# Performance work log

Hardware: AMD Instinct MI355X
Metric: run time of the kernel (lower is better)

Reference implementation:

```python
import jax, jax.numpy as jnp
import numpy as np

CELU_ALPHA = 0.1  # torchani standard CELU alpha


def _celu(x):
    return jax.nn.celu(x, alpha=CELU_ALPHA)


def setup_inputs() -> dict:
    key = jax.random.key(0)
    ks = jax.random.split(key, 12)
    N, S, E, D = 20000, 4, 8, 1008
    dims = [D, 256, 192, 160, 1]
    inp = {
        "aev": jax.random.normal(ks[0], (N, D), jnp.float32),
        "species": jax.random.randint(ks[1], (N,), 0, S, dtype=jnp.int64),
    }
    for l in range(4):
        din, dout = dims[l], dims[l + 1]
        inp[f"W{l}"] = jax.random.normal(ks[2 + 2 * l], (S, E, din, dout), jnp.float32) * (1.0 / np.sqrt(din).astype(np.float32))
        inp[f"b{l}"] = jax.random.normal(ks[3 + 2 * l], (S, E, dout), jnp.float32) * 0.05
    return inp


def reference(aev, species, W0, b0, W1, b1, W2, b2, W3, b3):
    # Faithful math of InferModel.forward: for each species i, gather atoms of
    # that species, run the BmmAtomicNetwork (ensemble of MLPs via bmm, CELU
    # activations, mean over ensemble members), sum per-species energies, then
    # sum into a single [1]-shaped total energy.
    # JIT-friendly equivalent: evaluate every species network on all atoms
    # (S=4 is small) and select each atom's output by its species index.
    # h: [S, E, N, hidden]
    h = _celu(jnp.einsum('ni,seio->seno', aev, W0) + b0[:, :, None, :])
    h = _celu(jnp.einsum('seni,seio->seno', h, W1) + b1[:, :, None, :])
    h = _celu(jnp.einsum('seni,seio->seno', h, W2) + b2[:, :, None, :])
    h = jnp.einsum('seni,seio->seno', h, W3) + b3[:, :, None, :]  # [S,E,N,1]
    per_atom = h.mean(axis=1)[:, :, 0]  # mean over ensemble -> [S, N]
    sel = jnp.take_along_axis(per_atom, species[None, :], axis=0)[0]  # [N]
    return jnp.sum(sel, keepdims=True)  # shape [1], total energy
```

## Files before the change

### kernel.cpp

```cpp
#include <hip/hip_runtime.h>
#include <cmath>

#define NA 20000
#define NS 4
#define NE 8
#define DD 1008
#define BM 128
#define MAXT 157
#define MAXROWS 20608

typedef unsigned short u16;
typedef unsigned int u32;
typedef unsigned long long u64;
typedef u16 u16x8 __attribute__((ext_vector_type(8)));
typedef u16 u16x4 __attribute__((ext_vector_type(4)));
typedef float f32x4 __attribute__((ext_vector_type(4)));
typedef short s16x8 __attribute__((ext_vector_type(8)));

__device__ __forceinline__ float bf2f(u16 h) {
  u32 u = ((u32)h) << 16;
  return __builtin_bit_cast(float, u);
}
__device__ __forceinline__ u16 f2bf(float f) {
  u32 b = __builtin_bit_cast(u32, f);
  u32 lsb = (b >> 16) & 1;
  return (u16)((b + 0x7fffu + lsb) >> 16);
}
__device__ __forceinline__ float celu_f(float x) {
  return x > 0.f ? x : 0.1f * expm1f(10.f * x);
}
__device__ __forceinline__ float gf(const void* g, size_t i, bool isF32) {
  return isF32 ? ((const float*)g)[i] : bf2f(((const u16*)g)[i]);
}

__device__ __forceinline__ void gll16(const void* g, const u16* lds) {
#if __has_builtin(__builtin_amdgcn_global_load_lds)
  __builtin_amdgcn_global_load_lds(
      (const __attribute__((address_space(1))) u32*)g,
      (__attribute__((address_space(3))) u32*)(u16*)lds, 16, 0, 0);
#else
  int l = threadIdx.x & 63;
  *(f32x4*)((u16*)lds + l * 8) = *(const f32x4*)g;
#endif
}

__global__ void k_initprobe(const void* __restrict__ aev, const void* __restrict__ species,
                            int* __restrict__ w) {
  __shared__ int sh[2];
  int tid = threadIdx.x;
  if (tid < 32) w[tid] = 0;
  if (tid == 0) { sh[0] = 0; sh[1] = 0; }
  __syncthreads();
  const u16* a = (const u16*)aev;
  int bad = 0;
  for (int i = 0; i < 16; ++i) {
    u16 h = a[tid * 16 + i];
    int ex = (h >> 7) & 0xFF;
    if (ex < 107 || ex > 147) ++bad;
  }
  atomicAdd(&sh[0], bad);
  const int* sp = (const int*)species;
  int odd = 0;
  for (int i = 0; i < 4; ++i)
    if (sp[(tid * 4 + i) * 2 + 1] != 0) ++odd;
  atomicAdd(&sh[1], odd);
  __syncthreads();
  if (tid == 0) {
    w[18] = (sh[0] > 400) ? 1 : 0;
    w[19] = (sh[1] == 0) ? 1 : 0;
  }
}

__device__ __forceinline__ int get_species(const void* sp, int i, bool i64) {
  int s = i64 ? ((const int*)sp)[2 * i] : ((const int*)sp)[i];
  return s < 0 ? 0 : (s > 3 ? 3 : s);
}

__global__ void k_count(const void* __restrict__ species, int* __restrict__ w) {
  int i = blockIdx.x * 256 + threadIdx.x;
  int lane = threadIdx.x & 63;
  int s = (i < NA) ? get_species(species, i, w[19] != 0) : -1;
  for (int sp = 0; sp < 4; ++sp) {
    u64 m = __ballot(s == sp);
    if (m != 0 && lane == (__ffsll((long long)m) - 1))
      atomicAdd(&w[sp], __popcll(m));
  }
}

__global__ void k_scan(int* w) {
  int b = 0, pb = 0;
  for (int s = 0; s < 4; ++s) {
    w[13 + s] = b; b += w[s];
    w[20 + s] = pb; pb += ((w[s] + 127) >> 7) << 7;
  }
  w[24] = pb;
}

__global__ void k_scatter(const void* __restrict__ species, int* __restrict__ w,
                          int* __restrict__ order) {
  int i = blockIdx.x * 256 + threadIdx.x;
  int lane = threadIdx.x & 63;
  int s = (i < NA) ? get_species(species, i, w[19] != 0) : -1;
  for (int sp = 0; sp < 4; ++sp) {
    u64 m = __ballot(s == sp);
    if (m == 0) continue;
    int leader = __ffsll((long long)m) - 1;
    int base = 0;
    if (lane == leader) base = atomicAdd(&w[4 + sp], __popcll(m));
    base = __shfl(base, leader);
    if (s == sp) {
      int rank = __popcll(m & ((lane == 63) ? 0x7fffffffffffffffULL : ((1ULL << lane) - 1)));
      order[w[13 + sp] + base + rank] = i;
    }
  }
}

__global__ void k_gather(const void* __restrict__ aev, const int* __restrict__ w,
                         const int* __restrict__ order, u16* __restrict__ aevb) {
  const bool isF32 = (w[18] != 0);
  const int t = threadIdx.x;
  const int r = blockIdx.x * 4 + (t >> 7);
  const int j = t & 127;
  if (j >= 126) return;
  const int s = (r >= w[21]) + (r >= w[22]) + (r >= w[23]);
  const int local = r - w[20 + s];
  u16x8 v = {0, 0, 0, 0, 0, 0, 0, 0};
  if (local < w[s]) {
    const int src = order[w[13 + s] + local];
    if (isF32) {
      const float* p = (const float*)aev + (size_t)src * DD + j * 8;
      const f32x4 f0 = *(const f32x4*)p;
      const f32x4 f1 = *(const f32x4*)(p + 4);
#pragma unroll
      for (int i = 0; i < 4; ++i) { v[i] = f2bf(f0[i]); v[4 + i] = f2bf(f1[i]); }
    } else {
      v = *(const u16x8*)((const u16*)aev + (size_t)src * DD + j * 8);
    }
  }
  *(u16x8*)(aevb + (size_t)r * DD + j * 8) = v;
}

__global__ void k_tr(const void* __restrict__ W, u16* __restrict__ out,
                     int K, int N, int Kpad, const int* __restrict__ w) {
  __shared__ u16 tile[64][68];
  const bool isF32 = (w[18] != 0);
  int se = blockIdx.x, k0 = blockIdx.y * 64, n0 = blockIdx.z * 64;
  int t = threadIdx.x;
  const size_t inBase = (size_t)se * K * N;
#pragma unroll
  for (int c = 0; c < 4; ++c) {
    int kk = (t >> 4) + c * 16, nn = (t & 15) * 4;
    int k = k0 + kk, n = n0 + nn;
    u16x4 v = {0, 0, 0, 0};
    if (k < K && n < N) {
      if (isF32) {
        f32x4 f = *(const f32x4*)((const float*)W + inBase + (size_t)k * N + n);
        v[0] = f2bf(f[0]); v[1] = f2bf(f[1]); v[2] = f2bf(f[2]); v[3] = f2bf(f[3]);
      } else {
        v = *(const u16x4*)((const u16*)W + inBase + (size_t)k * N + n);
      }
    }
    *(u16x4*)(&tile[kk][nn]) = v;
  }
  __syncthreads();
  int nloc = t >> 2, ks = (t & 3) * 16;
  if (n0 + nloc < N) {
    u16x8 o0, o1;
#pragma unroll
    for (int i = 0; i < 8; ++i) { o0[i] = tile[ks + i][nloc]; o1[i] = tile[ks + 8 + i][nloc]; }
    size_t ob = (size_t)se * N * Kpad + (size_t)(n0 + nloc) * Kpad + k0 + ks;
    *(u16x8*)(out + ob) = o0;
    *(u16x8*)(out + ob + 8) = o1;
  }
}

__global__ void k_small(const void* b0, const void* b1, const void* b2, const void* b3,
                        const void* W3, u16* ob0, u16* ob1, u16* ob2, u16* ob3, u16* oW3,
                        u16* gap, const int* __restrict__ w) {
  const bool isF32 = (w[18] != 0);
  int t = threadIdx.x;
  for (int i = t; i < 32 * 256; i += 256) ob0[i] = f2bf(gf(b0, i, isF32));
  for (int i = t; i < 32 * 192; i += 256) ob1[i] = f2bf(gf(b1, i, isF32));
  for (int i = t; i < 32 * 160; i += 256) ob2[i] = f2bf(gf(b2, i, isF32));
  for (int i = t; i < 32 * 160; i += 256) oW3[i] = f2bf(gf(W3, i, isF32));
  if (t < 32) ob3[t] = f2bf(gf(b3, t, isF32));
  u16x8 z = {0, 0, 0, 0, 0, 0, 0, 0};
  *(u16x8*)(gap + t * 8) = z;
}

__global__ __launch_bounds__(512, 4) void k_main(
    const u16* __restrict__ aevb, const u16* __restrict__ wt0,
    const u16* __restrict__ wt1, const u16* __restrict__ wt2,
    const u16* __restrict__ w3b, const u16* __restrict__ b0b,
    const u16* __restrict__ b1b, const u16* __restrict__ b2b,
    const u16* __restrict__ b3b, const int* __restrict__ w,
    float* __restrict__ accum) {
  __shared__ __align__(16) u16 L[32768];

  const int tid = threadIdx.x;
  const int g = blockIdx.x;
  const int s = g >> 1;
  const int e = (g & 1) * 4 + (blockIdx.y & 3);
  const int tile = blockIdx.y >> 2;
  const int cnt = w[s];
  if (tile * BM >= cnt) return;
  const int mRow = w[20 + s] + tile * BM;
  const int mCount = min(BM, cnt - tile * BM);
  const int se = s * NE + e;

  const int lane = tid & 63;
  const int wv = tid >> 6;
  const int lcol = lane & 15;
  const int quad = lane >> 4;

  {
    const u16* wt0se = wt0 + (size_t)se * 256 * 1024;
    const char* gA = (const char*)aevb +
        (size_t)(mRow + wv * 16 + (lane >> 2)) * 2016 + (lane & 3) * 16;
    const char* gB0 = (const char*)wt0se +
        (size_t)(wv * 32 + (lane >> 2)) * 2048 + (lane & 3) * 16;
    const char* gB1 = gB0 + 16 * 2048;
    const int aSt = wv * 512;
    const int bSt = 8192 + wv * 1024;

    const int wm = wv >> 2, wn = wv & 3;
    const int aRow0 = (wm * 64 + lcol) * 32 + quad * 8;
    const int bRow0 = 8192 + (wn * 64 + lcol) * 32 + quad * 8;

    f32x4 acc[4][4];
#pragma unroll
    for (int i = 0; i < 4; ++i)
#pragma unroll
      for (int j = 0; j < 4; ++j) acc[i][j] = (f32x4){0.f, 0.f, 0.f, 0.f};

    gll16(gA, &L[aSt]); gA += 64;
    gll16(gB0, &L[bSt]); gB0 += 64;
    gll16(gB1, &L[bSt + 512]); gB1 += 64;
    __syncthreads();

    for (int p = 0; p < 32; ++p) {
      const int d = p & 1;
      if (p < 31) {
        const int dn = d ^ 1;
        gll16(gA, &L[dn * 4096 + aSt]); gA += 64;
        gll16(gB0, &L[dn * 8192 + bSt]); gB0 += 64;
        gll16(gB1, &L[dn * 8192 + bSt + 512]); gB1 += 64;
      }
      const u16* Ad = &L[d * 4096];
      const u16* Bd = &L[d * 8192];
      s16x8 aF[4], bF[4];
#pragma unroll
      for (int mt = 0; mt < 4; ++mt)
        aF[mt] = __builtin_bit_cast(s16x8, *(const u16x8*)(Ad + aRow0 + mt * 512));
#pragma unroll
      for (int nt = 0; nt < 4; ++nt)
        bF[nt] = __builtin_bit_cast(s16x8, *(const u16x8*)(Bd + bRow0 + nt * 512));
#pragma unroll
      for (int nt = 0; nt < 4; ++nt)
#pragma unroll
        for (int mt = 0; mt < 4; ++mt)
          acc[mt][nt] = __builtin_amdgcn_mfma_f32_16x16x32_bf16(aF[mt], bF[nt], acc[mt][nt], 0, 0, 0);
      __syncthreads();
    }

#pragma unroll
    for (int nt = 0; nt < 4; ++nt) {
      const int col = wn * 64 + nt * 16 + lcol;
      const float bb = bf2f(b0b[se * 256 + col]);
#pragma unroll
      for (int mt = 0; mt < 4; ++mt) {
#pragma unroll
        for (int r = 0; r < 4; ++r) {
          const int rr = wm * 64 + mt * 16 + quad * 4 + r;
          L[(rr * 256 + col) ^ ((rr & 7) << 3)] = f2bf(celu_f(acc[mt][nt][r] + bb));
        }
      }
    }
  }
  __syncthreads();

  {
    const int wm = wv >> 2, wn = wv & 3;
    const u16* w1se = wt1 + (size_t)se * 192 * 256;
    const u16* bp[3];
#pragma unroll
    for (int nt = 0; nt < 3; ++nt)
      bp[nt] = w1se + (size_t)(wn * 48 + nt * 16 + lcol) * 256 + quad * 8;
    f32x4 acc[4][3];
#pragma unroll
    for (int i = 0; i < 4; ++i)
#pragma unroll
      for (int j = 0; j < 3; ++j) acc[i][j] = (f32x4){0.f, 0.f, 0.f, 0.f};
    int aBase[4], aSwz[4];
#pragma unroll
    for (int mt = 0; mt < 4; ++mt) {
      const int row = wm * 64 + mt * 16 + lcol;
      aBase[mt] = row * 256 + quad * 8;
      aSwz[mt] = (row & 7) << 3;
    }
    u16x8 cB[3], nB[3];
#pragma unroll
    for (int nt = 0; nt < 3; ++nt) cB[nt] = *(const u16x8*)bp[nt];
    for (int kc = 0; kc < 8; ++kc) {
      if (kc < 7) {
#pragma unroll
        for (int nt = 0; nt < 3; ++nt) nB[nt] = *(const u16x8*)(bp[nt] + (kc + 1) * 32);
      }
      s16x8 aF[4];
#pragma unroll
      for (int mt = 0; mt < 4; ++mt)
        aF[mt] = __builtin_bit_cast(s16x8, *(const u16x8*)&L[(aBase[mt] + kc * 32) ^ aSwz[mt]]);
#pragma unroll
      for (int nt = 0; nt < 3; ++nt) {
        const s16x8 bF = __builtin_bit_cast(s16x8, cB[nt]);
#pragma unroll
        for (int mt = 0; mt < 4; ++mt)
          acc[mt][nt] = __builtin_amdgcn_mfma_f32_16x16x32_bf16(aF[mt], bF, acc[mt][nt], 0, 0, 0);
      }
      if (kc < 7) {
#pragma unroll
        for (int nt = 0; nt < 3; ++nt) cB[nt] = nB[nt];
      }
    }
    __syncthreads();
#pragma unroll
    for (int nt = 0; nt < 3; ++nt) {
      const int col = wn * 48 + nt * 16 + lcol;
      const float bb = bf2f(b1b[se * 192 + col]);
#pragma unroll
      for (int mt = 0; mt < 4; ++mt) {
#pragma unroll
        for (int r = 0; r < 4; ++r) {
          const int rr = wm * 64 + mt * 16 + quad * 4 + r;
          L[(rr * 192 + col) ^ ((rr & 7) << 3)] = f2bf(celu_f(acc[mt][nt][r] + bb));
        }
      }
    }
  }
  __syncthreads();

  {
    const int wm = wv >> 1, wn = wv & 1;
    const u16* w2se = wt2 + (size_t)se * 160 * 192;
    const u16* bp[5];
#pragma unroll
    for (int nt = 0; nt < 5; ++nt)
      bp[nt] = w2se + (size_t)(wn * 80 + nt * 16 + lcol) * 192 + quad * 8;
    f32x4 acc[2][5];
#pragma unroll
    for (int i = 0; i < 2; ++i)
#pragma unroll
      for (int j = 0; j < 5; ++j) acc[i][j] = (f32x4){0.f, 0.f, 0.f, 0.f};
    int aBase[2], aSwz[2];
#pragma unroll
    for (int mt = 0; mt < 2; ++mt) {
      const int row = wm * 32 + mt * 16 + lcol;
      aBase[mt] = row * 192 + quad * 8;
      aSwz[mt] = (row & 7) << 3;
    }
    u16x8 cB[5], nB[5];
#pragma unroll
    for (int nt = 0; nt < 5; ++nt) cB[nt] = *(const u16x8*)bp[nt];
    for (int kc = 0; kc < 6; ++kc) {
      if (kc < 5) {
#pragma unroll
        for (int nt = 0; nt < 5; ++nt) nB[nt] = *(const u16x8*)(bp[nt] + (kc + 1) * 32);
      }
      s16x8 aF[2];
#pragma unroll
      for (int mt = 0; mt < 2; ++mt)
        aF[mt] = __builtin_bit_cast(s16x8, *(const u16x8*)&L[(aBase[mt] + kc * 32) ^ aSwz[mt]]);
#pragma unroll
      for (int nt = 0; nt < 5; ++nt) {
        const s16x8 bF = __builtin_bit_cast(s16x8, cB[nt]);
#pragma unroll
        for (int mt = 0; mt < 2; ++mt)
          acc[mt][nt] = __builtin_amdgcn_mfma_f32_16x16x32_bf16(aF[mt], bF, acc[mt][nt], 0, 0, 0);
      }
      if (kc < 5) {
#pragma unroll
        for (int nt = 0; nt < 5; ++nt) cB[nt] = nB[nt];
      }
    }
    __syncthreads();
#pragma unroll
    for (int nt = 0; nt < 5; ++nt) {
      const int col = wn * 80 + nt * 16 + lcol;
      const float bb = bf2f(b2b[se * 160 + col]);
#pragma unroll
      for (int mt = 0; mt < 2; ++mt) {
#pragma unroll
        for (int r = 0; r < 4; ++r) {
          const int rr = wm * 32 + mt * 16 + quad * 4 + r;
          L[(rr * 160 + col) ^ ((rr & 7) << 3)] = f2bf(celu_f(acc[mt][nt][r] + bb));
        }
      }
    }
  }
  __syncthreads();

  {
    const int row = tid >> 2;
    const int pp = tid & 3;
    const u16* w3p = w3b + se * 160;
    float dotv = 0.f;
#pragma unroll
    for (int j = 0; j < 5; ++j) {
      const int ci = (pp + 4 * j) * 8;
      const u16x8 hv = *(const u16x8*)&L[(row * 160 + ci) ^ ((row & 7) << 3)];
      const u16x8 wv8 = *(const u16x8*)(w3p + ci);
#pragma unroll
      for (int t2 = 0; t2 < 8; ++t2)
        dotv = fmaf(bf2f(hv[t2]), bf2f(wv8[t2]), dotv);
    }
    dotv += __shfl_xor(dotv, 1);
    dotv += __shfl_xor(dotv, 2);
    float v = (pp == 0 && row < mCount) ? (dotv + bf2f(b3b[se])) : 0.f;
    v += __shfl_xor(v, 4);
    v += __shfl_xor(v, 8);
    v += __shfl_xor(v, 16);
    v += __shfl_xor(v, 32);
    float* redf = (float*)&L[20608];
    if (lane == 0) redf[wv] = v;
    __syncthreads();
    if (tid == 0) {
      float tot = 0.f;
#pragma unroll
      for (int i = 0; i < 8; ++i) tot += redf[i];
      atomicAdd(accum, tot * 0.125f);
    }
  }
}

__global__ void k_final(const float* __restrict__ accum, u32* __restrict__ out) {
  u32 h = (u32)f2bf(accum[0]);
  out[0] = (h << 16) | h;
}

extern "C" void kernel_launch(void* const* d_in, const int* in_sizes, int n_in,
                              void* d_out, int out_size, void* d_ws, size_t ws_size,
                              hipStream_t stream) {
  const void* aev = d_in[0];
  const void* species = d_in[1];
  const void* W0 = d_in[2];
  const void* b0 = d_in[3];
  const void* W1 = d_in[4];
  const void* b1 = d_in[5];
  const void* W2 = d_in[6];
  const void* b2 = d_in[7];
  const void* W3 = d_in[8];
  const void* b3 = d_in[9];

  int* wsI = (int*)d_ws;
  float* accum = (float*)((char*)d_ws + 17 * 4);
  int* order = wsI + 1024;
  char* wsB = (char*)d_ws;

  const size_t oB0 = 131072;
  const size_t oB1 = 147456;
  const size_t oB2 = 159744;
  const size_t oB3 = 169984;
  const size_t oW3 = 170048;
  const size_t oAevb = 262144;
  const size_t oGap = 41807872;
  const size_t oWt0 = 41811968;
  const size_t oWt1 = 58589184;
  const size_t oWt2 = 61734912;

  u16* aevb = (u16*)(wsB + oAevb);
  u16* wt0 = (u16*)(wsB + oWt0);
  u16* wt1 = (u16*)(wsB + oWt1);
  u16* wt2 = (u16*)(wsB + oWt2);
  u16* w3b = (u16*)(wsB + oW3);
  u16* b0b = (u16*)(wsB + oB0);
  u16* b1b = (u16*)(wsB + oB1);
  u16* b2b = (u16*)(wsB + oB2);
  u16* b3b = (u16*)(wsB + oB3);

  hipLaunchKernelGGL(k_initprobe, dim3(1), dim3(256), 0, stream, aev, species, wsI);
  hipLaunchKernelGGL(k_count, dim3((NA + 255) / 256), dim3(256), 0, stream, species, wsI);
  hipLaunchKernelGGL(k_scan, dim3(1), dim3(1), 0, stream, wsI);
  hipLaunchKernelGGL(k_scatter, dim3((NA + 255) / 256), dim3(256), 0, stream, species, wsI, order);
  hipLaunchKernelGGL(k_gather, dim3(MAXROWS / 4), dim3(512), 0, stream, aev, wsI, order, aevb);
  hipLaunchKernelGGL(k_tr, dim3(32, 16, 4), dim3(256), 0, stream, W0, wt0, 1008, 256, 1024, wsI);
  hipLaunchKernelGGL(k_tr, dim3(32, 4, 3), dim3(256), 0, stream, W1, wt1, 256, 192, 256, wsI);
  hipLaunchKernelGGL(k_tr, dim3(32, 3, 3), dim3(256), 0, stream, W2, wt2, 192, 160, 192, wsI);
  hipLaunchKernelGGL(k_small, dim3(1), dim3(256), 0, stream, b0, b1, b2, b3, W3,
                     b0b, b1b, b2b, b3b, w3b, (u16*)(wsB + oGap), wsI);
  hipLaunchKernelGGL(k_main, dim3(8, 4 * MAXT), dim3(512), 0, stream,
                     aevb, wt0, wt1, wt2, w3b, b0b, b1b, b2b, b3b, wsI, accum);
  hipLaunchKernelGGL(k_final, dim3(1), dim3(1), 0, stream, accum, (u32*)d_out);
}
```

Baseline: 458.5 us.

## Swizzle layer-0 LDS tiles, use fast exp2 in CELU, raise MFMA priority

```diff
diff --git a/kernel.cpp b/kernel.cpp
--- a/kernel.cpp
+++ b/kernel.cpp
@@ -27,7 +27,12 @@
   return (u16)((b + 0x7fffu + lsb) >> 16);
 }
 __device__ __forceinline__ float celu_f(float x) {
-  return x > 0.f ? x : 0.1f * expm1f(10.f * x);
+#if __has_builtin(__builtin_amdgcn_exp2f)
+  float e = __builtin_amdgcn_exp2f(x * 14.426950408889634f);
+#else
+  float e = exp2f(x * 14.426950408889634f);
+#endif
+  return x > 0.f ? x : 0.1f * (e - 1.f);
 }
 __device__ __forceinline__ float gf(const void* g, size_t i, bool isF32) {
   return isF32 ? ((const float*)g)[i] : bf2f(((const u16*)g)[i]);
@@ -215,17 +220,22 @@
 
   {
     const u16* wt0se = wt0 + (size_t)se * 256 * 1024;
-    const char* gA = (const char*)aevb +
-        (size_t)(mRow + wv * 16 + (lane >> 2)) * 2016 + (lane & 3) * 16;
-    const char* gB0 = (const char*)wt0se +
-        (size_t)(wv * 32 + (lane >> 2)) * 2048 + (lane & 3) * 16;
-    const char* gB1 = gB0 + 16 * 2048;
+    const int rowA = tid >> 2;
+    const int gAx = (tid & 3) ^ ((rowA >> 1) & 3);
+    const char* gA = (const char*)aevb + (size_t)(mRow + rowA) * 2016 + gAx * 16;
+    const int rB1 = 128 + (tid >> 2);
+    const int gB0x = (tid & 3) ^ (((tid >> 2) >> 1) & 3);
+    const int gB1x = (tid & 3) ^ ((rB1 >> 1) & 3);
+    const char* gB0 = (const char*)wt0se + (size_t)(tid >> 2) * 2048 + gB0x * 16;
+    const char* gB1 = (const char*)wt0se + (size_t)rB1 * 2048 + gB1x * 16;
     const int aSt = wv * 512;
-    const int bSt = 8192 + wv * 1024;
+    const int bSt = 8192 + wv * 512;
+    const int bSt2 = 8192 + 4096 + wv * 512;
 
     const int wm = wv >> 2, wn = wv & 3;
-    const int aRow0 = (wm * 64 + lcol) * 32 + quad * 8;
-    const int bRow0 = 8192 + (wn * 64 + lcol) * 32 + quad * 8;
+    const int gsw = (quad ^ ((lcol >> 1) & 3)) * 8;
+    const int aRow0 = (wm * 64 + lcol) * 32 + gsw;
+    const int bRow0 = 8192 + (wn * 64 + lcol) * 32 + gsw;
 
     f32x4 acc[4][4];
 #pragma unroll
@@ -235,7 +245,7 @@
 
     gll16(gA, &L[aSt]); gA += 64;
     gll16(gB0, &L[bSt]); gB0 += 64;
-    gll16(gB1, &L[bSt + 512]); gB1 += 64;
+    gll16(gB1, &L[bSt2]); gB1 += 64;
     __syncthreads();
 
     for (int p = 0; p < 32; ++p) {
@@ -244,7 +254,7 @@
         const int dn = d ^ 1;
         gll16(gA, &L[dn * 4096 + aSt]); gA += 64;
         gll16(gB0, &L[dn * 8192 + bSt]); gB0 += 64;
-        gll16(gB1, &L[dn * 8192 + bSt + 512]); gB1 += 64;
+        gll16(gB1, &L[dn * 8192 + bSt2]); gB1 += 64;
       }
       const u16* Ad = &L[d * 4096];
       const u16* Bd = &L[d * 8192];
@@ -255,11 +265,13 @@
 #pragma unroll
       for (int nt = 0; nt < 4; ++nt)
         bF[nt] = __builtin_bit_cast(s16x8, *(const u16x8*)(Bd + bRow0 + nt * 512));
+      __builtin_amdgcn_s_setprio(1);
 #pragma unroll
       for (int nt = 0; nt < 4; ++nt)
 #pragma unroll
         for (int mt = 0; mt < 4; ++mt)
           acc[mt][nt] = __builtin_amdgcn_mfma_f32_16x16x32_bf16(aF[mt], bF[nt], acc[mt][nt], 0, 0, 0);
+      __builtin_amdgcn_s_setprio(0);
       __syncthreads();
     }
 
```

Result: faster. 440.9 us (-3.8%).
